# Optimization experiments

Measured on AMD Instinct MI355X. Metric: run time of the kernel, lower is better.

## Reference

```python
import jax, jax.numpy as jnp
import numpy as np

EMBED_DIM = 1024
HEAD_DIM = 64


def setup_inputs() -> dict:
    key = jax.random.key(0)
    ks = jax.random.split(key, 7)
    B, S = 4, 2048
    x = jax.random.normal(ks[0], (B, S, EMBED_DIM), dtype=jnp.float32)
    s = EMBED_DIM ** -0.5  # torch Linear default init scale (uniform bound)
    Wk = jax.random.uniform(ks[1], (EMBED_DIM, HEAD_DIM), minval=-s, maxval=s)
    bk = jax.random.uniform(ks[2], (HEAD_DIM,), minval=-s, maxval=s)
    Wq = jax.random.uniform(ks[3], (EMBED_DIM, HEAD_DIM), minval=-s, maxval=s)
    bq = jax.random.uniform(ks[4], (HEAD_DIM,), minval=-s, maxval=s)
    Wv = jax.random.uniform(ks[5], (EMBED_DIM, HEAD_DIM), minval=-s, maxval=s)
    bv = jax.random.uniform(ks[6], (HEAD_DIM,), minval=-s, maxval=s)
    return {"x": x, "Wq": Wq, "bq": bq, "Wk": Wk, "bk": bk, "Wv": Wv, "bv": bv}


def reference(x, Wq, bq, Wk, bk, Wv, bv):
    # projections: [B,S,D]
    q = x @ Wq + bq
    k = x @ Wk + bk
    v = x @ Wv + bv
    # NOTE: faithful to source, which DIVIDES by head_dim**-0.5 (i.e. multiplies by sqrt(d))
    scale = HEAD_DIM ** -0.5
    wei = jnp.einsum('bqd,bkd->bqk', q, k) / scale  # [B,S,S]
    S = x.shape[1]
    causal = jnp.tril(jnp.ones((S, S), dtype=bool))
    wei = jnp.where(causal, wei, -jnp.inf)
    attn_weights = jax.nn.softmax(wei, axis=-1)
    return jnp.einsum('bqk,bkd->bqd', attn_weights, v)
```

## Files before the change

kernel.cpp:

```cpp
#include <hip/hip_runtime.h>
#include <math.h>

#define S_LEN 2048
#define NB 4
#define EMB 1024
#define HD 64
#define NROW (NB * S_LEN)
#define NEG_BIG -3.0e38f
#define SC 11.5415603f
#define DEFER_THR 3.0f
#define KVSPLIT 4

typedef _Float16 half8 __attribute__((ext_vector_type(8)));
typedef _Float16 half4 __attribute__((ext_vector_type(4)));
typedef float f32x4 __attribute__((ext_vector_type(4)));

static __device__ __forceinline__ f32x4 mfma32(half8 a, half8 b, f32x4 c) {
    return __builtin_amdgcn_mfma_f32_16x16x32_f16(a, b, c, 0, 0, 0);
}
static __device__ __forceinline__ f32x4 mfma16(half4 a, half4 b, f32x4 c) {
    return __builtin_amdgcn_mfma_f32_16x16x16f16(a, b, c, 0, 0, 0);
}

__global__ __launch_bounds__(256) void prep_w(
    const float* __restrict__ Wq, const float* __restrict__ Wk,
    const float* __restrict__ Wv, _Float16* __restrict__ wt_frag)
{
    const int g  = blockIdx.x >> 4;
    const int kc = blockIdx.x & 15;
    const int k0 = kc * 64;
    const float* W = (g == 0) ? Wq : (g == 1) ? Wk : Wv;

    __shared__ float tile[64][68];
    const int t = threadIdx.x;
    {
        const int kk = t >> 2, cb = (t & 3) * 16;
#pragma unroll
        for (int i = 0; i < 4; i++)
            *(f32x4*)&tile[kk][cb + 4 * i] =
                *(const f32x4*)(W + (size_t)(k0 + kk) * HD + cb + 4 * i);
    }
    __syncthreads();

    const int c4 = t >> 6, l = t & 63;
    const int col = c4 * 16 + (l & 15);
    const int krow = (l >> 4) * 8;
#pragma unroll
    for (int sub = 0; sub < 2; sub++) {
        half8 hv;
#pragma unroll
        for (int e = 0; e < 8; e++)
            hv[e] = (_Float16)tile[sub * 32 + krow + e][col];
        const size_t addr = (size_t)(g * 4 + c4) * 16384 +
                            (size_t)(kc * 2 + sub) * 512 + (size_t)l * 8;
        *(half8*)(wt_frag + addr) = hv;
    }
}

__global__ __launch_bounds__(768) void proj_kernel(
    const float* __restrict__ x, const _Float16* __restrict__ wt_frag,
    const float* __restrict__ bq, const float* __restrict__ bk,
    const float* __restrict__ bv,
    _Float16* __restrict__ qs, _Float16* __restrict__ kh_,
    _Float16* __restrict__ vt)
{
    const int m0 = blockIdx.x * 32;
    const int t = threadIdx.x, lane = t & 63, w = t >> 6;

    __shared__ __align__(16) _Float16 xs[32][1032];

    for (int i = t; i < 4096; i += 768) {
        const int row = i >> 7, off = (i & 127) * 8;
        const float* xp = x + (size_t)(m0 + row) * EMB + off;
        const f32x4 v0 = *(const f32x4*)xp;
        const f32x4 v1 = *(const f32x4*)(xp + 4);
        half8 h;
#pragma unroll
        for (int jj = 0; jj < 4; jj++) {
            h[jj]     = (_Float16)v0[jj];
            h[4 + jj] = (_Float16)v1[jj];
        }
        *(half8*)&xs[row][off] = h;
    }

    const int f = w;
    const int row0 = lane & 15, kq = lane >> 4;
    const _Float16* wp = wt_frag + (size_t)f * 16384 + (size_t)lane * 8;

    half8 wbuf[4];
#pragma unroll
    for (int c = 0; c < 4; c++) wbuf[c] = *(const half8*)(wp + (size_t)c * 512);

    __syncthreads();

    f32x4 acc0 = f32x4{0, 0, 0, 0}, acc1 = f32x4{0, 0, 0, 0};

#pragma unroll
    for (int c = 0; c < 32; ++c) {
        const half8 ax0 = *(const half8*)&xs[row0][c * 32 + kq * 8];
        const half8 ax1 = *(const half8*)&xs[16 + row0][c * 32 + kq * 8];
        const half8 bw = wbuf[c & 3];
        acc0 = mfma32(ax0, bw, acc0);
        acc1 = mfma32(ax1, bw, acc1);
        if (c + 4 < 32) wbuf[c & 3] = *(const half8*)(wp + (size_t)(c + 4) * 512);
    }

    const int mat = f >> 2, c4 = f & 3;
    const int mcol = c4 * 16 + (lane & 15);
    const float bb = ((mat == 0) ? bq : (mat == 1) ? bk : bv)[mcol];
#pragma unroll
    for (int rh = 0; rh < 2; rh++) {
        const f32x4 acc = rh ? acc1 : acc0;
        const int grow0 = m0 + rh * 16 + kq * 4;
        if (mat == 0) {
#pragma unroll
            for (int r = 0; r < 4; r++)
                qs[(size_t)(grow0 + r) * HD + mcol] = (_Float16)((acc[r] + bb) * SC);
        } else if (mat == 1) {
#pragma unroll
            for (int r = 0; r < 4; r++)
                kh_[(size_t)(grow0 + r) * HD + mcol] = (_Float16)(acc[r] + bb);
        } else {
            half4 hv;
#pragma unroll
            for (int r = 0; r < 4; r++) hv[r] = (_Float16)(acc[r] + bb);
            const int bidx = grow0 >> 11, sr = grow0 & (S_LEN - 1);
            *(half4*)(vt + ((size_t)bidx * HD + mcol) * S_LEN + sr) = hv;
        }
    }
}

__global__ __launch_bounds__(512) void attn_kernel(
    const _Float16* __restrict__ qs, const _Float16* __restrict__ kh_,
    const _Float16* __restrict__ vt,
    float* __restrict__ po, float* __restrict__ pm, float* __restrict__ pl)
{
    const int id = blockIdx.x;
    const int qq = id & 3;
    const int b  = (id >> 2) & 3;
    const int qt = 31 - (id >> 4);
    const int q0 = qt * 64;
    const int t = threadIdx.x, lane = t & 63, w = t >> 6;
    const int rf = w >> 1, kvh = w & 1;

    __shared__ __align__(16) unsigned char smem[35840];
    _Float16 (*klds)[72] = (_Float16(*)[72])smem;
    _Float16 (*vlds)[72] = (_Float16(*)[72])(smem + 9216);
    float (*obuf)[16][68] = (float(*)[16][68])smem;
    float* mbuf = (float*)(smem + 34816);
    float* lbuf = (float*)(smem + 34816 + 512);

    const size_t rowq = ((size_t)b * S_LEN + q0 + rf * 16 + (lane & 15)) * HD + (lane >> 4) * 8;
    const half8 bq0 = *(const half8*)(qs + rowq);
    const half8 bq1 = *(const half8*)(qs + rowq + 32);

    f32x4 o[4];
#pragma unroll
    for (int c = 0; c < 4; c++) o[c] = f32x4{0, 0, 0, 0};
    float m_r = NEG_BIG, l_r = 0.f;

    const int nt = qt + 1;
    const int lo = (nt * qq) >> 2, hi = (nt * (qq + 1)) >> 2;

    const size_t kbase = (size_t)b * S_LEN * HD;
    const size_t vbase = (size_t)b * HD * S_LEN;
    const int srow = t >> 3, scol = (t & 7) * 8;

    half8 sK, sV;
    auto gload = [&](int tl) {
        sK = *(const half8*)(kh_ + kbase + (size_t)(tl * 64 + srow) * HD + scol);
        sV = *(const half8*)(vt + vbase + (size_t)srow * S_LEN + tl * 64 + scol);
    };
    auto swrite = [&]() {
        *(half8*)&klds[srow][scol] = sK;
        *(half8*)&vlds[srow][scol] = sV;
    };

    if (lo < hi) { gload(lo); swrite(); }
    __syncthreads();

    for (int tl = lo; tl < hi; ++tl) {
        if (tl + 1 < hi) gload(tl + 1);

        const int kv0 = tl * 64 + kvh * 32;
        __builtin_amdgcn_s_setprio(1);
        f32x4 s[2];
#pragma unroll
        for (int h = 0; h < 2; h++) {
            const int keyl = kvh * 32 + 16 * h + (lane & 15);
            f32x4 a = f32x4{0, 0, 0, 0};
            a = mfma32(*(const half8*)&klds[keyl][(lane >> 4) * 8], bq0, a);
            a = mfma32(*(const half8*)&klds[keyl][32 + (lane >> 4) * 8], bq1, a);
            s[h] = a;
        }
        __builtin_amdgcn_s_setprio(0);

        const int qrow = q0 + rf * 16 + (lane & 15);
        const int kb0  = kv0 + (lane >> 4) * 4;
        float tv[8];
#pragma unroll
        for (int h = 0; h < 2; h++)
#pragma unroll
            for (int r = 0; r < 4; r++)
                tv[h * 4 + r] = (kb0 + 16 * h + r <= qrow) ? s[h][r] : NEG_BIG;

        float mt = tv[0];
#pragma unroll
        for (int i = 1; i < 8; i++) mt = fmaxf(mt, tv[i]);
        mt = fmaxf(mt, __shfl_xor(mt, 16));
        mt = fmaxf(mt, __shfl_xor(mt, 32));

        if (!__all(mt <= m_r + DEFER_THR)) {
            const float mn = fmaxf(m_r, mt);
            const float corr = exp2f(m_r - mn);
            m_r = mn;
            l_r *= corr;
            float corrB[4];
#pragma unroll
            for (int r = 0; r < 4; r++) corrB[r] = __shfl(corr, (lane >> 4) * 4 + r);
#pragma unroll
            for (int c = 0; c < 4; c++)
#pragma unroll
                for (int r = 0; r < 4; r++) o[c][r] *= corrB[r];
        }

        float p[8], rs = 0.f;
#pragma unroll
        for (int i = 0; i < 8; i++) { p[i] = exp2f(tv[i] - m_r); rs += p[i]; }
        rs += __shfl_xor(rs, 16);
        rs += __shfl_xor(rs, 32);
        l_r += rs;

        half4 pa[2];
#pragma unroll
        for (int h = 0; h < 2; h++)
#pragma unroll
            for (int r = 0; r < 4; r++) pa[h][r] = (_Float16)p[h * 4 + r];
        __builtin_amdgcn_s_setprio(1);
#pragma unroll
        for (int c = 0; c < 4; c++) {
#pragma unroll
            for (int h = 0; h < 2; h++) {
                const half4 vf = *(const half4*)&vlds[16 * c + (lane & 15)]
                                                    [kvh * 32 + 16 * h + (lane >> 4) * 4];
                o[c] = mfma16(pa[h], vf, o[c]);
            }
        }
        __builtin_amdgcn_s_setprio(0);

        __syncthreads();
        if (tl + 1 < hi) swrite();
        __syncthreads();
    }

    if (lane < 16) { mbuf[w * 16 + lane] = m_r; lbuf[w * 16 + lane] = l_r; }
#pragma unroll
    for (int c = 0; c < 4; c++)
#pragma unroll
        for (int r = 0; r < 4; r++)
            obuf[w][(lane >> 4) * 4 + r][16 * c + (lane & 15)] = o[c][r];
    __syncthreads();

    if (t < 256) {
        const int row16 = t >> 4, cb = (t & 15) * 4;
#pragma unroll
        for (int rf2 = 0; rf2 < 4; rf2++) {
            const int w0 = rf2 * 2, w1 = w0 + 1;
            const float m0v = mbuf[w0 * 16 + row16], m1v = mbuf[w1 * 16 + row16];
            const float M = fmaxf(m0v, m1v);
            const float e0 = exp2f(m0v - M), e1 = exp2f(m1v - M);
            const float L = lbuf[w0 * 16 + row16] * e0 + lbuf[w1 * 16 + row16] * e1;
            const f32x4 o0 = *(const f32x4*)&obuf[w0][row16][cb];
            const f32x4 o1 = *(const f32x4*)&obuf[w1][row16][cb];
            f32x4 acc;
#pragma unroll
            for (int jj = 0; jj < 4; jj++) acc[jj] = o0[jj] * e0 + o1[jj] * e1;
            const size_t idx = (size_t)(qq * NB + b) * S_LEN + q0 + rf2 * 16 + row16;
            *(f32x4*)(po + idx * HD + cb) = acc;
            if ((t & 15) == 0) { pm[idx] = M; pl[idx] = L; }
        }
    }
}

__global__ __launch_bounds__(256) void merge_kernel(
    const float* __restrict__ po, const float* __restrict__ pm,
    const float* __restrict__ pl, float* __restrict__ out)
{
    const int b = blockIdx.y;
    const int row = blockIdx.x * 16 + (threadIdx.x >> 4);
    const int cb = (threadIdx.x & 15) * 4;

    float mv[KVSPLIT];
    float M = NEG_BIG;
#pragma unroll
    for (int qq = 0; qq < KVSPLIT; qq++) {
        mv[qq] = pm[(size_t)(qq * NB + b) * S_LEN + row];
        M = fmaxf(M, mv[qq]);
    }
    float L = 0.f;
    f32x4 acc = f32x4{0, 0, 0, 0};
#pragma unroll
    for (int qq = 0; qq < KVSPLIT; qq++) {
        const size_t idx = (size_t)(qq * NB + b) * S_LEN + row;
        const float e = exp2f(mv[qq] - M);
        L += pl[idx] * e;
        const f32x4 ov = *(const f32x4*)(po + idx * HD + cb);
#pragma unroll
        for (int jj = 0; jj < 4; jj++) acc[jj] += ov[jj] * e;
    }
    const float inv = 1.0f / L;
    f32x4 res;
#pragma unroll
    for (int jj = 0; jj < 4; jj++) res[jj] = acc[jj] * inv;
    *(f32x4*)(out + ((size_t)b * S_LEN + row) * HD + cb) = res;
}

extern "C" void kernel_launch(void* const* d_in, const int* in_sizes, int n_in,
                              void* d_out, int out_size, void* d_ws, size_t ws_size,
                              hipStream_t stream) {
    const float* x  = (const float*)d_in[0];
    const float* Wq = (const float*)d_in[1];
    const float* bq = (const float*)d_in[2];
    const float* Wk = (const float*)d_in[3];
    const float* bk = (const float*)d_in[4];
    const float* Wv = (const float*)d_in[5];
    const float* bv = (const float*)d_in[6];
    float* out = (float*)d_out;

    _Float16* ws = (_Float16*)d_ws;
    const size_t nW = (size_t)192 * EMB;
    const size_t n  = (size_t)NROW * HD;
    _Float16* wt_frag = ws;
    _Float16* qsb = wt_frag + nW;
    _Float16* khb = qsb + n;
    _Float16* vtb = khb + n;
    float* po = (float*)(vtb + n);
    float* pm = po + (size_t)KVSPLIT * NB * S_LEN * HD;
    float* pl = pm + (size_t)KVSPLIT * NB * S_LEN;

    prep_w<<<48, 256, 0, stream>>>(Wq, Wk, Wv, wt_frag);
    proj_kernel<<<NROW / 32, 768, 0, stream>>>(
        x, wt_frag, bq, bk, bv, qsb, khb, vtb);
    attn_kernel<<<32 * NB * KVSPLIT, 512, 0, stream>>>(qsb, khb, vtb, po, pm, pl);
    merge_kernel<<<dim3(S_LEN / 16, NB), 256, 0, stream>>>(po, pm, pl, out);
}
```

Before: 38.83 us.

## Double-buffer K/V tiles in LDS and store split-KV partials as fp16

The attention loop now keeps two K/V tile buffers in LDS, writing the next tile into the alternate buffer, which removes one of the two barriers per iteration. Separately, the per-split partial outputs are stored as fp16 instead of fp32, halving the traffic between the attention kernel and the merge kernel. LDS use per block grows slightly. The fp16 partials lose some precision, though they are unnormalized values bounded by the row sum.

Measured after the change: 36.73 us. 1.06x faster.

```diff
diff --git a/kernel.cpp b/kernel.cpp
--- a/kernel.cpp
+++ b/kernel.cpp
@@ -133,7 +133,7 @@
 __global__ __launch_bounds__(512) void attn_kernel(
     const _Float16* __restrict__ qs, const _Float16* __restrict__ kh_,
     const _Float16* __restrict__ vt,
-    float* __restrict__ po, float* __restrict__ pm, float* __restrict__ pl)
+    _Float16* __restrict__ po, float* __restrict__ pm, float* __restrict__ pl)
 {
     const int id = blockIdx.x;
     const int qq = id & 3;
@@ -143,12 +143,12 @@
     const int t = threadIdx.x, lane = t & 63, w = t >> 6;
     const int rf = w >> 1, kvh = w & 1;
 
-    __shared__ __align__(16) unsigned char smem[35840];
-    _Float16 (*klds)[72] = (_Float16(*)[72])smem;
-    _Float16 (*vlds)[72] = (_Float16(*)[72])(smem + 9216);
+    __shared__ __align__(16) unsigned char smem[37888];
+    _Float16 (*klds)[64][72] = (_Float16(*)[64][72])smem;
+    _Float16 (*vlds)[64][72] = (_Float16(*)[64][72])(smem + 18432);
     float (*obuf)[16][68] = (float(*)[16][68])smem;
-    float* mbuf = (float*)(smem + 34816);
-    float* lbuf = (float*)(smem + 34816 + 512);
+    float* mbuf = (float*)(smem + 36864);
+    float* lbuf = (float*)(smem + 36864 + 512);
 
     const size_t rowq = ((size_t)b * S_LEN + q0 + rf * 16 + (lane & 15)) * HD + (lane >> 4) * 8;
     const half8 bq0 = *(const half8*)(qs + rowq);
@@ -171,14 +171,15 @@
         sK = *(const half8*)(kh_ + kbase + (size_t)(tl * 64 + srow) * HD + scol);
         sV = *(const half8*)(vt + vbase + (size_t)srow * S_LEN + tl * 64 + scol);
     };
-    auto swrite = [&]() {
-        *(half8*)&klds[srow][scol] = sK;
-        *(half8*)&vlds[srow][scol] = sV;
+    auto swrite = [&](int nb) {
+        *(half8*)&klds[nb][srow][scol] = sK;
+        *(half8*)&vlds[nb][srow][scol] = sV;
     };
 
-    if (lo < hi) { gload(lo); swrite(); }
+    if (lo < hi) { gload(lo); swrite(0); }
     __syncthreads();
 
+    int cur = 0;
     for (int tl = lo; tl < hi; ++tl) {
         if (tl + 1 < hi) gload(tl + 1);
 
@@ -189,8 +190,8 @@
         for (int h = 0; h < 2; h++) {
             const int keyl = kvh * 32 + 16 * h + (lane & 15);
             f32x4 a = f32x4{0, 0, 0, 0};
-            a = mfma32(*(const half8*)&klds[keyl][(lane >> 4) * 8], bq0, a);
-            a = mfma32(*(const half8*)&klds[keyl][32 + (lane >> 4) * 8], bq1, a);
+            a = mfma32(*(const half8*)&klds[cur][keyl][(lane >> 4) * 8], bq0, a);
+            a = mfma32(*(const half8*)&klds[cur][keyl][32 + (lane >> 4) * 8], bq1, a);
             s[h] = a;
         }
         __builtin_amdgcn_s_setprio(0);
@@ -241,16 +242,16 @@
         for (int c = 0; c < 4; c++) {
 #pragma unroll
             for (int h = 0; h < 2; h++) {
-                const half4 vf = *(const half4*)&vlds[16 * c + (lane & 15)]
+                const half4 vf = *(const half4*)&vlds[cur][16 * c + (lane & 15)]
                                                     [kvh * 32 + 16 * h + (lane >> 4) * 4];
                 o[c] = mfma16(pa[h], vf, o[c]);
             }
         }
         __builtin_amdgcn_s_setprio(0);
 
+        if (tl + 1 < hi) swrite(cur ^ 1);
         __syncthreads();
-        if (tl + 1 < hi) swrite();
-        __syncthreads();
+        cur ^= 1;
     }
 
     if (lane < 16) { mbuf[w * 16 + lane] = m_r; lbuf[w * 16 + lane] = l_r; }
@@ -272,18 +273,18 @@
             const float L = lbuf[w0 * 16 + row16] * e0 + lbuf[w1 * 16 + row16] * e1;
             const f32x4 o0 = *(const f32x4*)&obuf[w0][row16][cb];
             const f32x4 o1 = *(const f32x4*)&obuf[w1][row16][cb];
-            f32x4 acc;
-#pragma unroll
-            for (int jj = 0; jj < 4; jj++) acc[jj] = o0[jj] * e0 + o1[jj] * e1;
+            half4 hv;
+#pragma unroll
+            for (int jj = 0; jj < 4; jj++) hv[jj] = (_Float16)(o0[jj] * e0 + o1[jj] * e1);
             const size_t idx = (size_t)(qq * NB + b) * S_LEN + q0 + rf2 * 16 + row16;
-            *(f32x4*)(po + idx * HD + cb) = acc;
+            *(half4*)(po + idx * HD + cb) = hv;
             if ((t & 15) == 0) { pm[idx] = M; pl[idx] = L; }
         }
     }
 }
 
 __global__ __launch_bounds__(256) void merge_kernel(
-    const float* __restrict__ po, const float* __restrict__ pm,
+    const _Float16* __restrict__ po, const float* __restrict__ pm,
     const float* __restrict__ pl, float* __restrict__ out)
 {
     const int b = blockIdx.y;
@@ -304,9 +305,9 @@
         const size_t idx = (size_t)(qq * NB + b) * S_LEN + row;
         const float e = exp2f(mv[qq] - M);
         L += pl[idx] * e;
-        const f32x4 ov = *(const f32x4*)(po + idx * HD + cb);
-#pragma unroll
-        for (int jj = 0; jj < 4; jj++) acc[jj] += ov[jj] * e;
+        const half4 ov = *(const half4*)(po + idx * HD + cb);
+#pragma unroll
+        for (int jj = 0; jj < 4; jj++) acc[jj] += (float)ov[jj] * e;
     }
     const float inv = 1.0f / L;
     f32x4 res;
@@ -334,8 +335,8 @@
     _Float16* qsb = wt_frag + nW;
     _Float16* khb = qsb + n;
     _Float16* vtb = khb + n;
-    float* po = (float*)(vtb + n);
-    float* pm = po + (size_t)KVSPLIT * NB * S_LEN * HD;
+    _Float16* po = vtb + n;
+    float* pm = (float*)(po + (size_t)KVSPLIT * NB * S_LEN * HD);
     float* pl = pm + (size_t)KVSPLIT * NB * S_LEN;
 
     prep_w<<<48, 256, 0, stream>>>(Wq, Wk, Wv, wt_frag);
```
